# Optimization experiments

Measured on AMD Instinct MI355X. Metric: run time of the kernel, lower is better.

## Reference

```python
import jax, jax.numpy as jnp
import numpy as np

E, H, NH, FFN, OUT = 4096, 512, 4, 1024, 1
HD = H // NH
LN_EPS = 1e-5


def setup_inputs() -> dict:
    key = jax.random.key(0)
    ks = jax.random.split(key, 20)
    s = 1.0 / np.sqrt(H)
    inp = {
        'x': jax.random.normal(ks[0], (E, H), jnp.float32),
        'edge_index': jax.random.randint(ks[1], (2, E), 0, E, jnp.int64),
        # DMPNN message linear
        'W_msg': jax.random.normal(ks[2], (H, H), jnp.float32) * s,
        'b_msg': jnp.zeros((H,), jnp.float32),
        # GRUCell weights (torch layout: [3H, H], gates r,z,n)
        'W_ih': jax.random.normal(ks[3], (3 * H, H), jnp.float32) * s,
        'b_ih': jnp.zeros((3 * H,), jnp.float32),
        'W_hh': jax.random.normal(ks[4], (3 * H, H), jnp.float32) * s,
        'b_hh': jnp.zeros((3 * H,), jnp.float32),
        # MultiheadAttention combined in-proj [3H, H] and out-proj [H, H]
        'W_in_proj': jax.random.normal(ks[5], (3 * H, H), jnp.float32) * s,
        'b_in_proj': jnp.zeros((3 * H,), jnp.float32),
        'W_out_proj': jax.random.normal(ks[6], (H, H), jnp.float32) * s,
        'b_out_proj': jnp.zeros((H,), jnp.float32),
        # LayerNorm
        'ln_g': jnp.ones((H,), jnp.float32),
        'ln_b': jnp.zeros((H,), jnp.float32),
        # GlobalAttention output linear
        'W_lin': jax.random.normal(ks[7], (H, H), jnp.float32) * s,
        'b_lin': jnp.zeros((H,), jnp.float32),
        # FFN: Linear(H->FFN), ReLU, Linear(FFN->OUT)
        'W_f1': jax.random.normal(ks[8], (FFN, H), jnp.float32) * s,
        'b_f1': jnp.zeros((FFN,), jnp.float32),
        'W_f2': jax.random.normal(ks[9], (OUT, FFN), jnp.float32) * (1.0 / np.sqrt(FFN)),
        'b_f2': jnp.zeros((OUT,), jnp.float32),
    }
    return inp


def reference(x, edge_index, W_msg, b_msg, W_ih, b_ih, W_hh, b_hh,
              W_in_proj, b_in_proj, W_out_proj, b_out_proj, ln_g, ln_b,
              W_lin, b_lin, W_f1, b_f1, W_f2, b_f2):
    # ---- DMPNNLayer: message + scatter-add aggregation + GRUCell update ----
    msg = jax.nn.relu(x @ W_msg.T + b_msg)                       # [E, H]
    agg = jnp.zeros_like(x).at[edge_index[1]].add(msg)           # scatter-add to dst edges
    gi = agg @ W_ih.T + b_ih                                     # [E, 3H]
    gh = x @ W_hh.T + b_hh                                       # [E, 3H]
    ir, iz, inn = jnp.split(gi, 3, axis=-1)
    hr, hz, hn = jnp.split(gh, 3, axis=-1)
    r = jax.nn.sigmoid(ir + hr)
    z = jax.nn.sigmoid(iz + hz)
    n = jnp.tanh(inn + r * hn)
    h = (1.0 - z) * n + z * x                                    # [E, H] updated edges
    # ---- GlobalAttention: MHA(h,h,h) + residual LN + relu(linear) ----
    qkv = h @ W_in_proj.T + b_in_proj                            # [E, 3H]
    q, k, v = jnp.split(qkv, 3, axis=-1)
    split_heads = lambda t: t.reshape(E, NH, HD).transpose(1, 0, 2)  # [NH, E, HD]
    q, k, v = split_heads(q), split_heads(k), split_heads(v)
    scale = np.float32(1.0 / np.sqrt(HD))
    attn = jax.nn.softmax(jnp.einsum('hqd,hkd->hqk', q, k) * scale, axis=-1)
    o = jnp.einsum('hqk,hkd->hqd', attn, v).transpose(1, 0, 2).reshape(E, H)
    o = o @ W_out_proj.T + b_out_proj
    y = o + h
    mu = jnp.mean(y, axis=-1, keepdims=True)
    var = jnp.mean((y - mu) ** 2, axis=-1, keepdims=True)
    yn = (y - mu) / jnp.sqrt(var + LN_EPS) * ln_g + ln_b
    g = jax.nn.relu(yn @ W_lin.T + b_lin)                        # [E, H]
    # ---- FFN ----
    f = jax.nn.relu(g @ W_f1.T + b_f1)                           # [E, FFN]
    return f @ W_f2.T + b_f2                                     # [E, OUT]
```

## Files before the change

### kernel.cpp

```cpp
#include <hip/hip_runtime.h>

typedef unsigned short ushort_t;
typedef __attribute__((ext_vector_type(8))) short short8;
typedef __attribute__((ext_vector_type(4))) float float4v;

#define E_N   4096
#define H_N   512
#define NH_N  4
#define HD_N  128
#define FFN_N 1024
#define H3_N  1536

__device__ __forceinline__ float bf2f(ushort_t u) {
  union { unsigned u; float f; } v; v.u = ((unsigned)u) << 16; return v.f;
}
__device__ __forceinline__ ushort_t f2bf(float f) {
  union { float f; unsigned u; } v; v.f = f;
  unsigned r = v.u + 0x7fffu + ((v.u >> 16) & 1u);
  return (ushort_t)(r >> 16);
}
__device__ __forceinline__ uint4 cvt8(const float* p) {
  float4 a = *(const float4*)p;
  float4 b = *(const float4*)(p + 4);
  union { ushort_t u[8]; uint4 v; } pk;
  pk.u[0] = f2bf(a.x); pk.u[1] = f2bf(a.y); pk.u[2] = f2bf(a.z); pk.u[3] = f2bf(a.w);
  pk.u[4] = f2bf(b.x); pk.u[5] = f2bf(b.y); pk.u[6] = f2bf(b.z); pk.u[7] = f2bf(b.w);
  return pk.v;
}
__device__ __forceinline__ uint4 cvt8v(float4 a, float4 b) {
  union { ushort_t u[8]; uint4 v; } pk;
  pk.u[0] = f2bf(a.x); pk.u[1] = f2bf(a.y); pk.u[2] = f2bf(a.z); pk.u[3] = f2bf(a.w);
  pk.u[4] = f2bf(b.x); pk.u[5] = f2bf(b.y); pk.u[6] = f2bf(b.z); pk.u[7] = f2bf(b.w);
  return pk.v;
}

__device__ __forceinline__ void gload16(const void* g, void* l) {
  __builtin_amdgcn_global_load_lds(
      (const __attribute__((address_space(1))) unsigned*)g,
      (__attribute__((address_space(3))) unsigned*)l, 16, 0, 0);
}

__global__ __launch_bounds__(256) void prep_kernel(
    const float* __restrict__ wmsg, const float* __restrict__ wih,
    const float* __restrict__ whh,  const float* __restrict__ win,
    const float* __restrict__ wout, const float* __restrict__ wlin,
    const float* __restrict__ wf1,  ushort_t* __restrict__ wdst,
    float4* __restrict__ agg, const float* __restrict__ b2,
    float* __restrict__ out)
{
  int b = blockIdx.x;
  if (b < 2048) {
    agg[(size_t)b * 256 + threadIdx.x] = make_float4(0.f, 0.f, 0.f, 0.f);
    return;
  }
  if (b < 3840) {
    size_t o = ((size_t)(b - 2048) * 256 + threadIdx.x) * 8;
    const float* s;
    if      (o <  262144) s = wmsg + o;
    else if (o < 1048576) s = wih  + (o -  262144);
    else if (o < 1835008) s = whh  + (o - 1048576);
    else if (o < 2621440) s = win  + (o - 1835008);
    else if (o < 2883584) s = wout + (o - 2621440);
    else if (o < 3145728) s = wlin + (o - 2883584);
    else                  s = wf1  + (o - 3145728);
    *(uint4*)(wdst + o) = cvt8(s);
    return;
  }
  int i = (b - 3840) * 256 + threadIdx.x;
  out[i] = b2[0];
}

enum { MODE_MSG = 0, MODE_GI = 1, MODE_GH = 2, MODE_QKV = 3, MODE_OUT = 4,
       MODE_LIN = 5, MODE_F1 = 6 };

template <int MODE, int ASRC>
__global__ __launch_bounds__(256, 3) void gemm_bt(
    const void* __restrict__ Av, const ushort_t* __restrict__ W,
    const float* __restrict__ bias, int K,
    float* __restrict__ outf, ushort_t* __restrict__ outb,
    const int* __restrict__ edge, float* __restrict__ aggf,
    const ushort_t* __restrict__ hres,
    ushort_t* __restrict__ qb, ushort_t* __restrict__ kb,
    ushort_t* __restrict__ vt, const float* __restrict__ wf2)
{
  __shared__ ushort_t As[2][128 * 64];
  __shared__ ushort_t Bs[2][64 * 64];
  char* AsB = (char*)As;
  char* BsB = (char*)Bs;

  const int tid  = threadIdx.x;
  const int lane = tid & 63;
  const int wave = tid >> 6;
  const int quad = lane >> 4;
  const int l15  = lane & 15;
  const int m0 = blockIdx.x * 128;
  const int n0 = blockIdx.y * 64;
  const int wm = (wave >> 1) * 64;
  const int wn = (wave & 1) * 32;

  float4v acc[4][2];
#pragma unroll
  for (int i = 0; i < 4; i++)
#pragma unroll
    for (int j = 0; j < 2; j++)
#pragma unroll
      for (int r = 0; r < 4; r++) acc[i][j][r] = 0.f;

  const int ar = tid >> 3;
  const int ac = (tid & 7) * 8;
  const int awb = (ac * 2) ^ ((ar & 7) << 4);
  const int rmask = (l15 & 7) << 4;

  uint4  pa[4], pb[2];
  float4 fa[8];

#define LOADA(KK)                                                              \
  do {                                                                         \
    if constexpr (ASRC == 0) {                                                 \
      const ushort_t* Ab = (const ushort_t*)Av;                                \
      _Pragma("unroll")                                                        \
      for (int i = 0; i < 4; i++)                                              \
        pa[i] = *(const uint4*)(Ab + (size_t)(m0 + ar + 32 * i) * K + (KK) + ac); \
    } else {                                                                   \
      const float* Af = (const float*)Av;                                      \
      _Pragma("unroll")                                                        \
      for (int i = 0; i < 4; i++) {                                            \
        const float* p = Af + (size_t)(m0 + ar + 32 * i) * K + (KK) + ac;      \
        fa[2 * i]     = *(const float4*)(p);                                   \
        fa[2 * i + 1] = *(const float4*)(p + 4);                               \
      }                                                                        \
    }                                                                          \
  } while (0)

#define LOADB(KK)                                                              \
  do {                                                                         \
    _Pragma("unroll")                                                          \
    for (int i = 0; i < 2; i++)                                                \
      pb[i] = *(const uint4*)(W + (size_t)(n0 + ar + 32 * i) * K + (KK) + ac); \
  } while (0)

#define WRITEAB(BUF)                                                           \
  do {                                                                         \
    _Pragma("unroll")                                                          \
    for (int i = 0; i < 4; i++) {                                              \
      uint4 v_;                                                                \
      if constexpr (ASRC == 0) v_ = pa[i];                                     \
      else                     v_ = cvt8v(fa[2 * i], fa[2 * i + 1]);           \
      *(uint4*)(AsB + (BUF) * 16384 + (ar + 32 * i) * 128 + awb) = v_;         \
    }                                                                          \
    _Pragma("unroll")                                                          \
    for (int i = 0; i < 2; i++)                                                \
      *(uint4*)(BsB + (BUF) * 8192 + (ar + 32 * i) * 128 + awb) = pb[i];       \
  } while (0)

  LOADA(0);
  LOADB(0);
  WRITEAB(0);
  int cur = 0;

  for (int k0 = 0; k0 < K; k0 += 64) {
    const bool more = (k0 + 64 < K);
    if (more) { LOADA(k0 + 64); LOADB(k0 + 64); }
    __syncthreads();

#pragma unroll
    for (int ks = 0; ks < 2; ks++) {
      short8 af[4], bfr[2];
#pragma unroll
      for (int i = 0; i < 4; i++)
        af[i] = *(const short8*)(AsB + cur * 16384 +
                 (wm + i * 16 + l15) * 128 + ((ks * 64 + quad * 16) ^ rmask));
#pragma unroll
      for (int j = 0; j < 2; j++)
        bfr[j] = *(const short8*)(BsB + cur * 8192 +
                 (wn + j * 16 + l15) * 128 + ((ks * 64 + quad * 16) ^ rmask));
#pragma unroll
      for (int i = 0; i < 4; i++)
#pragma unroll
        for (int j = 0; j < 2; j++)
          acc[i][j] = __builtin_amdgcn_mfma_f32_16x16x32_bf16(af[i], bfr[j],
                                                              acc[i][j], 0, 0, 0);
    }

    if (more) WRITEAB(cur ^ 1);
    cur ^= 1;
  }
#undef LOADA
#undef LOADB
#undef WRITEAB

  if constexpr (MODE == MODE_F1) {
    float fsum[4][4];
#pragma unroll
    for (int i = 0; i < 4; i++)
#pragma unroll
      for (int r = 0; r < 4; r++) fsum[i][r] = 0.f;
#pragma unroll
    for (int j = 0; j < 2; j++) {
      const int col = n0 + wn + j * 16 + l15;
      const float bv = bias[col];
      const float wv = wf2[col];
#pragma unroll
      for (int i = 0; i < 4; i++)
#pragma unroll
        for (int r = 0; r < 4; r++)
          fsum[i][r] += fmaxf(acc[i][j][r] + bv, 0.f) * wv;
    }
#pragma unroll
    for (int i = 0; i < 4; i++)
#pragma unroll
      for (int r = 0; r < 4; r++) {
        float s = fsum[i][r];
        s += __shfl_xor(s, 1, 64); s += __shfl_xor(s, 2, 64);
        s += __shfl_xor(s, 4, 64); s += __shfl_xor(s, 8, 64);
        if (l15 == 0)
          atomicAdd(&outf[m0 + wm + i * 16 + quad * 4 + r], s);
      }
  } else {
#pragma unroll
    for (int j = 0; j < 2; j++) {
      const int col = n0 + wn + j * 16 + l15;
      const float bv = bias[col];
#pragma unroll
      for (int i = 0; i < 4; i++) {
#pragma unroll
        for (int r = 0; r < 4; r++) {
          const int row = m0 + wm + i * 16 + quad * 4 + r;
          float v = acc[i][j][r] + bv;
          if constexpr (MODE == MODE_MSG) {
            v = fmaxf(v, 0.f);
            const int dst = edge[E_N + row] & (E_N - 1);
            atomicAdd(&aggf[(size_t)dst * H_N + col], v);
          } else if constexpr (MODE == MODE_GI || MODE == MODE_GH) {
            outb[(size_t)row * H3_N + col] = f2bf(v);
          } else if constexpr (MODE == MODE_QKV) {
            const int part = col >> 9;
            const int hh   = (col >> 7) & 3;
            const int d    = col & 127;
            const ushort_t bvv = f2bf(v);
            if (part == 0)      qb[((size_t)hh * E_N + row) * HD_N + d] = bvv;
            else if (part == 1) kb[((size_t)hh * E_N + row) * HD_N + d] = bvv;
            else                vt[((size_t)hh * HD_N + d) * E_N + row] = bvv;
          } else if constexpr (MODE == MODE_OUT) {
            v += bf2f(hres[(size_t)row * H_N + col]);
            outf[(size_t)row * H_N + col] = v;
          } else {
            outb[(size_t)row * H_N + col] = f2bf(fmaxf(v, 0.f));
          }
        }
      }
    }
  }
}

__global__ __launch_bounds__(512, 2) void attn_kernel(
    const ushort_t* __restrict__ Qg, const ushort_t* __restrict__ Kg,
    const ushort_t* __restrict__ Vtg, ushort_t* __restrict__ Ob)
{
  const int bid  = blockIdx.x;
  const int head = bid & 3;
  const int qb0  = (bid >> 2) * 64;
  const int tid  = threadIdx.x;
  const int wave = tid >> 6;
  const int grp  = wave >> 2;
  const int w4   = wave & 3;
  const int lane = tid & 63;
  const int quad = lane >> 4;
  const int l15  = lane & 15;

  __shared__ ushort_t Ks[2][2][64][128];
  __shared__ ushort_t Vs[2][2][128][64];
  __shared__ ushort_t Ps[8][16][64];
  char* Psc = (char*)Ps + wave * 2048;

  const ushort_t* Qhead  = Qg  + (size_t)head * E_N * HD_N;
  const ushort_t* Khead  = Kg  + (size_t)head * E_N * HD_N;
  const ushort_t* Vthead = Vtg + (size_t)head * HD_N * E_N;

  short8 aq[4];
#pragma unroll
  for (int ks = 0; ks < 4; ks++)
    aq[ks] = *(const short8*)(Qhead +
        (size_t)(qb0 + w4 * 16 + l15) * HD_N + ks * 32 + quad * 8);

  float4v oacc[8];
#pragma unroll
  for (int i = 0; i < 8; i++)
#pragma unroll
    for (int r = 0; r < 4; r++) oacc[i][r] = 0.f;
  float mprev[4], lsum[4];
#pragma unroll
  for (int r = 0; r < 4; r++) { mprev[r] = -1e30f; lsum[r] = 0.f; }

  const float scale = 0.088388347648318447f;
  const int q15sw = (l15 & 7) << 4;

  const int kt0 = grp * 2048;

#define ISSUE(KT, BUF)                                                         \
  do {                                                                         \
    char* kb_ = (char*)Ks + ((grp * 2 + (BUF)) << 14);                         \
    char* vb_ = (char*)Vs + ((grp * 2 + (BUF)) << 14);                         \
    _Pragma("unroll")                                                          \
    for (int i_ = 0; i_ < 4; i_++) {                                           \
      const int c_ = w4 * 4 + i_;                                              \
      const int krow_ = 4 * c_ + (lane >> 4);              \
      gload16(Khead + (size_t)((KT) + krow_) * HD_N +                          \
                  (((((lane & 15) * 16)) ^ ((krow_ & 7) << 4)) >> 1),          \
              kb_ + c_ * 1024);                                                \
      const int vrow_ = 8 * c_ + (lane >> 3);             \
      gload16(Vthead + (size_t)vrow_ * E_N + (KT) +                            \
                  (((((lane & 7) * 16)) ^ ((lane >> 3) << 4)) >> 1),           \
              vb_ + c_ * 1024);                                                \
    }                                                                          \
  } while (0)

  ISSUE(kt0, 0);
  int cur = 0;

  for (int it = 0; it < 32; it++) {
    __syncthreads();
    if (it + 1 < 32) ISSUE(kt0 + (it + 1) * 64, cur ^ 1);

    const char* kt_ = (char*)Ks + ((grp * 2 + cur) << 14);
    const char* vt_ = (char*)Vs + ((grp * 2 + cur) << 14);

    float4v sacc[4];
#pragma unroll
    for (int j = 0; j < 4; j++)
#pragma unroll
      for (int r = 0; r < 4; r++) sacc[j][r] = 0.f;
#pragma unroll
    for (int ks = 0; ks < 4; ks++) {
#pragma unroll
      for (int j = 0; j < 4; j++) {
        short8 bk = *(const short8*)(kt_ + (j * 16 + l15) * 256 +
                                     ((ks * 64 + quad * 16) ^ q15sw));
        sacc[j] = __builtin_amdgcn_mfma_f32_16x16x32_bf16(aq[ks], bk, sacc[j], 0, 0, 0);
      }
    }

    float alpha[4], pv[4][4];
#pragma unroll
    for (int r = 0; r < 4; r++) {
      float mx = -1e30f;
#pragma unroll
      for (int j = 0; j < 4; j++) { float s = sacc[j][r] * scale; pv[j][r] = s; mx = fmaxf(mx, s); }
#pragma unroll
      for (int off = 1; off < 16; off <<= 1) mx = fmaxf(mx, __shfl_xor(mx, off, 64));
      float mnew = fmaxf(mprev[r], mx);
      alpha[r] = __expf(mprev[r] - mnew);
      float ss = 0.f;
#pragma unroll
      for (int j = 0; j < 4; j++) { float p = __expf(pv[j][r] - mnew); pv[j][r] = p; ss += p; }
#pragma unroll
      for (int off = 1; off < 16; off <<= 1) ss += __shfl_xor(ss, off, 64);
      lsum[r] = lsum[r] * alpha[r] + ss;
      mprev[r] = mnew;
    }
#pragma unroll
    for (int i = 0; i < 8; i++)
#pragma unroll
      for (int r = 0; r < 4; r++) oacc[i][r] *= alpha[r];

#pragma unroll
    for (int j = 0; j < 4; j++)
#pragma unroll
      for (int r = 0; r < 4; r++) {
        const int prow = quad * 4 + r;
        *(ushort_t*)(Psc + prow * 128 +
                     ((2 * (j * 16 + l15)) ^ ((prow & 7) << 4))) = f2bf(pv[j][r]);
      }

#pragma unroll
    for (int ks2 = 0; ks2 < 2; ks2++) {
      short8 ap = *(const short8*)(Psc + l15 * 128 +
                                   ((ks2 * 64 + quad * 16) ^ q15sw));
#pragma unroll
      for (int j = 0; j < 8; j++) {
        short8 bv = *(const short8*)(vt_ + (j * 16 + l15) * 128 +
                                     ((ks2 * 64 + quad * 16) ^ q15sw));
        oacc[j] = __builtin_amdgcn_mfma_f32_16x16x32_bf16(ap, bv, oacc[j], 0, 0, 0);
      }
    }
    cur ^= 1;
  }
#undef ISSUE

  __syncthreads();
  float* mO  = (float*)Ks;
  float* mML = (float*)Vs;
  if (grp == 1) {
#pragma unroll
    for (int j = 0; j < 8; j++)
#pragma unroll
      for (int r = 0; r < 4; r++)
        mO[(w4 * 16 + quad * 4 + r) * 128 + j * 16 + l15] = oacc[j][r];
    if (l15 == 0) {
#pragma unroll
      for (int r = 0; r < 4; r++) {
        mML[(w4 * 16 + quad * 4 + r) * 2 + 0] = mprev[r];
        mML[(w4 * 16 + quad * 4 + r) * 2 + 1] = lsum[r];
      }
    }
  }
  __syncthreads();
  if (grp == 0) {
    float s0[4], s1[4];
#pragma unroll
    for (int r = 0; r < 4; r++) {
      int rr = w4 * 16 + quad * 4 + r;
      float m1 = mML[rr * 2 + 0], l1 = mML[rr * 2 + 1];
      float m  = fmaxf(mprev[r], m1);
      float e0 = __expf(mprev[r] - m);
      float e1 = __expf(m1 - m);
      float inv = 1.f / (lsum[r] * e0 + l1 * e1);
      s0[r] = e0 * inv;
      s1[r] = e1 * inv;
    }
#pragma unroll
    for (int j = 0; j < 8; j++)
#pragma unroll
      for (int r = 0; r < 4; r++) {
        int row = qb0 + w4 * 16 + quad * 4 + r;
        int col = head * HD_N + j * 16 + l15;
        float o1 = mO[(w4 * 16 + quad * 4 + r) * 128 + j * 16 + l15];
        Ob[(size_t)row * H_N + col] = f2bf(oacc[j][r] * s0[r] + o1 * s1[r]);
      }
  }
}

__global__ __launch_bounds__(256) void gru_kernel(
    const ushort_t* __restrict__ gib, const ushort_t* __restrict__ ghb,
    const float* __restrict__ x, ushort_t* __restrict__ hb) {
  int t = blockIdx.x * 256 + threadIdx.x;
  int e = t >> 6, j8 = (t & 63) * 8;
  size_t b = (size_t)e * H3_N + j8;
  short8 vir = *(const short8*)(gib + b);
  short8 viz = *(const short8*)(gib + b + 512);
  short8 vin = *(const short8*)(gib + b + 1024);
  short8 vhr = *(const short8*)(ghb + b);
  short8 vhz = *(const short8*)(ghb + b + 512);
  short8 vhn = *(const short8*)(ghb + b + 1024);
  size_t xo = (size_t)e * H_N + j8;
  float4 x0 = *(const float4*)(x + xo);
  float4 x1 = *(const float4*)(x + xo + 4);
  float xv[8] = {x0.x, x0.y, x0.z, x0.w, x1.x, x1.y, x1.z, x1.w};
  union { ushort_t u[8]; uint4 v; } o;
#pragma unroll
  for (int i = 0; i < 8; i++) {
    float ir = bf2f((ushort_t)vir[i]), iz = bf2f((ushort_t)viz[i]), inn = bf2f((ushort_t)vin[i]);
    float hr = bf2f((ushort_t)vhr[i]), hz = bf2f((ushort_t)vhz[i]), hn  = bf2f((ushort_t)vhn[i]);
    float r = 1.f / (1.f + __expf(-(ir + hr)));
    float z = 1.f / (1.f + __expf(-(iz + hz)));
    float n = tanhf(inn + r * hn);
    o.u[i] = f2bf((1.f - z) * n + z * xv[i]);
  }
  *(uint4*)(hb + xo) = o.v;
}

__global__ __launch_bounds__(256) void ln_kernel(
    const float* __restrict__ y, const float* __restrict__ g,
    const float* __restrict__ b, ushort_t* __restrict__ yn) {
  int wave = threadIdx.x >> 6, lane = threadIdx.x & 63;
  int row = blockIdx.x * 4 + wave;
  const float* yr = y + (size_t)row * H_N;
  float v[8], s = 0.f;
#pragma unroll
  for (int i = 0; i < 8; i++) { v[i] = yr[lane + i * 64]; s += v[i]; }
#pragma unroll
  for (int off = 1; off < 64; off <<= 1) s += __shfl_xor(s, off, 64);
  float mu = s * (1.f / 512.f);
  float q = 0.f;
#pragma unroll
  for (int i = 0; i < 8; i++) { float d = v[i] - mu; q += d * d; }
#pragma unroll
  for (int off = 1; off < 64; off <<= 1) q += __shfl_xor(q, off, 64);
  float rstd = rsqrtf(q * (1.f / 512.f) + 1e-5f);
#pragma unroll
  for (int i = 0; i < 8; i++) {
    int c = lane + i * 64;
    yn[(size_t)row * H_N + c] = f2bf((v[i] - mu) * rstd * g[c] + b[c]);
  }
}

extern "C" void kernel_launch(void* const* d_in, const int* in_sizes, int n_in,
                              void* d_out, int out_size, void* d_ws, size_t ws_size,
                              hipStream_t stream) {
  const float* x     = (const float*)d_in[0];
  const int*   edge  = (const int*)d_in[1];
  const float* W_msg = (const float*)d_in[2];
  const float* b_msg = (const float*)d_in[3];
  const float* W_ih  = (const float*)d_in[4];
  const float* b_ih  = (const float*)d_in[5];
  const float* W_hh  = (const float*)d_in[6];
  const float* b_hh  = (const float*)d_in[7];
  const float* W_in  = (const float*)d_in[8];
  const float* b_in  = (const float*)d_in[9];
  const float* W_out = (const float*)d_in[10];
  const float* b_out = (const float*)d_in[11];
  const float* ln_g  = (const float*)d_in[12];
  const float* ln_b  = (const float*)d_in[13];
  const float* W_lin = (const float*)d_in[14];
  const float* b_lin = (const float*)d_in[15];
  const float* W_f1  = (const float*)d_in[16];
  const float* b_f1  = (const float*)d_in[17];
  const float* W_f2  = (const float*)d_in[18];
  const float* b_f2  = (const float*)d_in[19];

  char* ws = (char*)d_ws;
  const size_t MB = 1024 * 1024;
  float*    agg = (float*)(ws + 1 * MB);
  ushort_t* hb  = (ushort_t*)(ws + 1 * MB);
  ushort_t* gib = (ushort_t*)(ws + 9 * MB);
  ushort_t* ghb = (ushort_t*)(ws + 21 * MB);
  ushort_t* Qb  = (ushort_t*)(ws + 5 * MB);
  ushort_t* Kb  = (ushort_t*)(ws + 9 * MB);
  ushort_t* Vt  = (ushort_t*)(ws + 13 * MB);
  ushort_t* ob  = (ushort_t*)(ws + 17 * MB);
  float*    y   = (float*)(ws + 21 * MB);
  ushort_t* ynb = (ushort_t*)(ws + 29 * MB);
  ushort_t* gb  = (ushort_t*)(ws + 31 * MB);
  ushort_t* wbf = (ushort_t*)(ws + 33 * MB);
  ushort_t* Wmsg_b = wbf;
  ushort_t* Wih_b  = wbf + 262144;
  ushort_t* Whh_b  = wbf + 1048576;
  ushort_t* Win_b  = wbf + 1835008;
  ushort_t* Wout_b = wbf + 2621440;
  ushort_t* Wlin_b = wbf + 2883584;
  ushort_t* Wf1_b  = wbf + 3145728;

  prep_kernel<<<3856, 256, 0, stream>>>(
      W_msg, W_ih, W_hh, W_in, W_out, W_lin, W_f1, wbf,
      (float4*)agg, b_f2, (float*)d_out);

  gemm_bt<MODE_MSG, 1><<<dim3(32, 8), 256, 0, stream>>>(
      x, Wmsg_b, b_msg, H_N, nullptr, nullptr, edge, agg, nullptr,
      nullptr, nullptr, nullptr, nullptr);

  gemm_bt<MODE_GI, 1><<<dim3(32, 24), 256, 0, stream>>>(
      agg, Wih_b, b_ih, H_N, nullptr, gib, nullptr, nullptr, nullptr,
      nullptr, nullptr, nullptr, nullptr);

  gemm_bt<MODE_GH, 1><<<dim3(32, 24), 256, 0, stream>>>(
      x, Whh_b, b_hh, H_N, nullptr, ghb, nullptr, nullptr, nullptr,
      nullptr, nullptr, nullptr, nullptr);

  gru_kernel<<<1024, 256, 0, stream>>>(gib, ghb, x, hb);

  gemm_bt<MODE_QKV, 0><<<dim3(32, 24), 256, 0, stream>>>(
      hb, Win_b, b_in, H_N, nullptr, nullptr, nullptr, nullptr, nullptr,
      Qb, Kb, Vt, nullptr);

  attn_kernel<<<256, 512, 0, stream>>>(Qb, Kb, Vt, ob);

  gemm_bt<MODE_OUT, 0><<<dim3(32, 8), 256, 0, stream>>>(
      ob, Wout_b, b_out, H_N, y, nullptr, nullptr, nullptr, hb,
      nullptr, nullptr, nullptr, nullptr);

  ln_kernel<<<1024, 256, 0, stream>>>(y, ln_g, ln_b, ynb);

  gemm_bt<MODE_LIN, 0><<<dim3(32, 8), 256, 0, stream>>>(
      ynb, Wlin_b, b_lin, H_N, nullptr, gb, nullptr, nullptr, nullptr,
      nullptr, nullptr, nullptr, nullptr);

  gemm_bt<MODE_F1, 0><<<dim3(32, 16), 256, 0, stream>>>(
      gb, Wf1_b, b_f1, H_N, (float*)d_out, nullptr, nullptr, nullptr, nullptr,
      nullptr, nullptr, nullptr, W_f2);
}
```

Measured before the change: 340.3 us.

## Stage GEMM tiles via direct global-to-LDS loads with bf16 A inputs and BM=64 tiles

The GEMM now loads tiles with global_load_lds straight into swizzled LDS instead of going through registers. For that to work, every A operand must already be bf16, so x is converted in the prep kernel and agg gets its own conversion kernel. The narrow-N GEMMs (msg, out, lin) switch to a 64-row tile with twice as many blocks to raise occupancy. The cost is an extra kernel launch and the extra conversion traffic for x and agg.

```diff
diff --git a/kernel.cpp b/kernel.cpp
--- a/kernel.cpp
+++ b/kernel.cpp
@@ -27,12 +27,6 @@
   pk.u[4] = f2bf(b.x); pk.u[5] = f2bf(b.y); pk.u[6] = f2bf(b.z); pk.u[7] = f2bf(b.w);
   return pk.v;
 }
-__device__ __forceinline__ uint4 cvt8v(float4 a, float4 b) {
-  union { ushort_t u[8]; uint4 v; } pk;
-  pk.u[0] = f2bf(a.x); pk.u[1] = f2bf(a.y); pk.u[2] = f2bf(a.z); pk.u[3] = f2bf(a.w);
-  pk.u[4] = f2bf(b.x); pk.u[5] = f2bf(b.y); pk.u[6] = f2bf(b.z); pk.u[7] = f2bf(b.w);
-  return pk.v;
-}
 
 __device__ __forceinline__ void gload16(const void* g, void* l) {
   __builtin_amdgcn_global_load_lds(
@@ -41,10 +35,11 @@
 }
 
 __global__ __launch_bounds__(256) void prep_kernel(
+    const float* __restrict__ x,
     const float* __restrict__ wmsg, const float* __restrict__ wih,
     const float* __restrict__ whh,  const float* __restrict__ win,
     const float* __restrict__ wout, const float* __restrict__ wlin,
-    const float* __restrict__ wf1,  ushort_t* __restrict__ wdst,
+    const float* __restrict__ wf1,  ushort_t* __restrict__ dst,
     float4* __restrict__ agg, const float* __restrict__ b2,
     float* __restrict__ out)
 {
@@ -53,29 +48,36 @@
     agg[(size_t)b * 256 + threadIdx.x] = make_float4(0.f, 0.f, 0.f, 0.f);
     return;
   }
-  if (b < 3840) {
+  if (b < 4864) {
     size_t o = ((size_t)(b - 2048) * 256 + threadIdx.x) * 8;
     const float* s;
-    if      (o <  262144) s = wmsg + o;
-    else if (o < 1048576) s = wih  + (o -  262144);
-    else if (o < 1835008) s = whh  + (o - 1048576);
-    else if (o < 2621440) s = win  + (o - 1835008);
-    else if (o < 2883584) s = wout + (o - 2621440);
-    else if (o < 3145728) s = wlin + (o - 2883584);
-    else                  s = wf1  + (o - 3145728);
-    *(uint4*)(wdst + o) = cvt8(s);
+    if      (o < 2097152) s = x    + o;
+    else if (o < 2359296) s = wmsg + (o - 2097152);
+    else if (o < 3145728) s = wih  + (o - 2359296);
+    else if (o < 3932160) s = whh  + (o - 3145728);
+    else if (o < 4718592) s = win  + (o - 3932160);
+    else if (o < 4980736) s = wout + (o - 4718592);
+    else if (o < 5242880) s = wlin + (o - 4980736);
+    else                  s = wf1  + (o - 5242880);
+    *(uint4*)(dst + o) = cvt8(s);
     return;
   }
-  int i = (b - 3840) * 256 + threadIdx.x;
+  int i = (b - 4864) * 256 + threadIdx.x;
   out[i] = b2[0];
+}
+
+__global__ __launch_bounds__(256) void cvt_agg_kernel(
+    const float* __restrict__ agg, ushort_t* __restrict__ aggb) {
+  size_t o = ((size_t)blockIdx.x * 256 + threadIdx.x) * 8;
+  *(uint4*)(aggb + o) = cvt8(agg + o);
 }
 
 enum { MODE_MSG = 0, MODE_GI = 1, MODE_GH = 2, MODE_QKV = 3, MODE_OUT = 4,
        MODE_LIN = 5, MODE_F1 = 6 };
 
-template <int MODE, int ASRC>
-__global__ __launch_bounds__(256, 3) void gemm_bt(
-    const void* __restrict__ Av, const ushort_t* __restrict__ W,
+template <int MODE, int BM>
+__global__ __launch_bounds__(256, (BM == 64 ? 2 : 3)) void gemm_bt(
+    const ushort_t* __restrict__ A, const ushort_t* __restrict__ W,
     const float* __restrict__ bias, int K,
     float* __restrict__ outf, ushort_t* __restrict__ outb,
     const int* __restrict__ edge, float* __restrict__ aggf,
@@ -83,116 +85,87 @@
     ushort_t* __restrict__ qb, ushort_t* __restrict__ kb,
     ushort_t* __restrict__ vt, const float* __restrict__ wf2)
 {
-  __shared__ ushort_t As[2][128 * 64];
+  constexpr int MI   = BM / 32;
+  constexpr int ASZ  = BM * 128;
+  constexpr int BSZ  = 64 * 128;
+  constexpr int NCHA = BM / 8;
+  constexpr int NCH  = NCHA + 8;
+
+  __shared__ ushort_t As[2][BM * 64];
   __shared__ ushort_t Bs[2][64 * 64];
-  char* AsB = (char*)As;
-  char* BsB = (char*)Bs;
 
   const int tid  = threadIdx.x;
   const int lane = tid & 63;
   const int wave = tid >> 6;
   const int quad = lane >> 4;
   const int l15  = lane & 15;
-  const int m0 = blockIdx.x * 128;
+  const int m0 = blockIdx.x * BM;
   const int n0 = blockIdx.y * 64;
-  const int wm = (wave >> 1) * 64;
+  const int wm = (wave >> 1) * (BM / 2);
   const int wn = (wave & 1) * 32;
-
-  float4v acc[4][2];
-#pragma unroll
-  for (int i = 0; i < 4; i++)
+  const int rmask = (l15 & 7) << 4;
+
+  const int crow  = lane >> 3;
+  const int selem = ((((lane & 7) * 16)) ^ (crow << 4)) >> 1;
+
+  float4v acc[MI][2];
+#pragma unroll
+  for (int i = 0; i < MI; i++)
 #pragma unroll
     for (int j = 0; j < 2; j++)
 #pragma unroll
       for (int r = 0; r < 4; r++) acc[i][j][r] = 0.f;
 
-  const int ar = tid >> 3;
-  const int ac = (tid & 7) * 8;
-  const int awb = (ac * 2) ^ ((ar & 7) << 4);
-  const int rmask = (l15 & 7) << 4;
-
-  uint4  pa[4], pb[2];
-  float4 fa[8];
-
-#define LOADA(KK)                                                              \
+#define ISSUE(KK, BUF)                                                         \
   do {                                                                         \
-    if constexpr (ASRC == 0) {                                                 \
-      const ushort_t* Ab = (const ushort_t*)Av;                                \
-      _Pragma("unroll")                                                        \
-      for (int i = 0; i < 4; i++)                                              \
-        pa[i] = *(const uint4*)(Ab + (size_t)(m0 + ar + 32 * i) * K + (KK) + ac); \
-    } else {                                                                   \
-      const float* Af = (const float*)Av;                                      \
-      _Pragma("unroll")                                                        \
-      for (int i = 0; i < 4; i++) {                                            \
-        const float* p = Af + (size_t)(m0 + ar + 32 * i) * K + (KK) + ac;      \
-        fa[2 * i]     = *(const float4*)(p);                                   \
-        fa[2 * i + 1] = *(const float4*)(p + 4);                               \
+    _Pragma("unroll")                                                          \
+    for (int j_ = 0; j_ < NCH / 4; j_++) {                                     \
+      const int c_ = wave + j_ * 4;                                            \
+      if (c_ < NCHA) {                                                         \
+        const int row_ = c_ * 8 + crow;                                        \
+        gload16(A + (size_t)(m0 + row_) * K + (KK) + selem,                    \
+                (char*)As + (BUF) * ASZ + c_ * 1024);                          \
+      } else {                                                                 \
+        const int row_ = (c_ - NCHA) * 8 + crow;                               \
+        gload16(W + (size_t)(n0 + row_) * K + (KK) + selem,                    \
+                (char*)Bs + (BUF) * BSZ + (c_ - NCHA) * 1024);                 \
       }                                                                        \
     }                                                                          \
   } while (0)
 
-#define LOADB(KK)                                                              \
-  do {                                                                         \
-    _Pragma("unroll")                                                          \
-    for (int i = 0; i < 2; i++)                                                \
-      pb[i] = *(const uint4*)(W + (size_t)(n0 + ar + 32 * i) * K + (KK) + ac); \
-  } while (0)
-
-#define WRITEAB(BUF)                                                           \
-  do {                                                                         \
-    _Pragma("unroll")                                                          \
-    for (int i = 0; i < 4; i++) {                                              \
-      uint4 v_;                                                                \
-      if constexpr (ASRC == 0) v_ = pa[i];                                     \
-      else                     v_ = cvt8v(fa[2 * i], fa[2 * i + 1]);           \
-      *(uint4*)(AsB + (BUF) * 16384 + (ar + 32 * i) * 128 + awb) = v_;         \
-    }                                                                          \
-    _Pragma("unroll")                                                          \
-    for (int i = 0; i < 2; i++)                                                \
-      *(uint4*)(BsB + (BUF) * 8192 + (ar + 32 * i) * 128 + awb) = pb[i];       \
-  } while (0)
-
-  LOADA(0);
-  LOADB(0);
-  WRITEAB(0);
+  ISSUE(0, 0);
   int cur = 0;
 
   for (int k0 = 0; k0 < K; k0 += 64) {
-    const bool more = (k0 + 64 < K);
-    if (more) { LOADA(k0 + 64); LOADB(k0 + 64); }
     __syncthreads();
+    if (k0 + 64 < K) ISSUE(k0 + 64, cur ^ 1);
 
 #pragma unroll
     for (int ks = 0; ks < 2; ks++) {
-      short8 af[4], bfr[2];
-#pragma unroll
-      for (int i = 0; i < 4; i++)
-        af[i] = *(const short8*)(AsB + cur * 16384 +
+      short8 af[MI], bfr[2];
+#pragma unroll
+      for (int i = 0; i < MI; i++)
+        af[i] = *(const short8*)((char*)As + cur * ASZ +
                  (wm + i * 16 + l15) * 128 + ((ks * 64 + quad * 16) ^ rmask));
 #pragma unroll
       for (int j = 0; j < 2; j++)
-        bfr[j] = *(const short8*)(BsB + cur * 8192 +
+        bfr[j] = *(const short8*)((char*)Bs + cur * BSZ +
                  (wn + j * 16 + l15) * 128 + ((ks * 64 + quad * 16) ^ rmask));
 #pragma unroll
-      for (int i = 0; i < 4; i++)
+      for (int i = 0; i < MI; i++)
 #pragma unroll
         for (int j = 0; j < 2; j++)
           acc[i][j] = __builtin_amdgcn_mfma_f32_16x16x32_bf16(af[i], bfr[j],
                                                               acc[i][j], 0, 0, 0);
     }
-
-    if (more) WRITEAB(cur ^ 1);
     cur ^= 1;
   }
-#undef LOADA
-#undef LOADB
-#undef WRITEAB
+#undef ISSUE
 
   if constexpr (MODE == MODE_F1) {
-    float fsum[4][4];
-#pragma unroll
-    for (int i = 0; i < 4; i++)
+    float fsum[MI][4];
+#pragma unroll
+    for (int i = 0; i < MI; i++)
 #pragma unroll
       for (int r = 0; r < 4; r++) fsum[i][r] = 0.f;
 #pragma unroll
@@ -201,13 +174,13 @@
       const float bv = bias[col];
       const float wv = wf2[col];
 #pragma unroll
-      for (int i = 0; i < 4; i++)
+      for (int i = 0; i < MI; i++)
 #pragma unroll
         for (int r = 0; r < 4; r++)
           fsum[i][r] += fmaxf(acc[i][j][r] + bv, 0.f) * wv;
     }
 #pragma unroll
-    for (int i = 0; i < 4; i++)
+    for (int i = 0; i < MI; i++)
 #pragma unroll
       for (int r = 0; r < 4; r++) {
         float s = fsum[i][r];
@@ -222,7 +195,7 @@
       const int col = n0 + wn + j * 16 + l15;
       const float bv = bias[col];
 #pragma unroll
-      for (int i = 0; i < 4; i++) {
+      for (int i = 0; i < MI; i++) {
 #pragma unroll
         for (int r = 0; r < 4; r++) {
           const int row = m0 + wm + i * 16 + quad * 4 + r;
@@ -510,61 +483,64 @@
 
   char* ws = (char*)d_ws;
   const size_t MB = 1024 * 1024;
-  float*    agg = (float*)(ws + 1 * MB);
-  ushort_t* hb  = (ushort_t*)(ws + 1 * MB);
-  ushort_t* gib = (ushort_t*)(ws + 9 * MB);
-  ushort_t* ghb = (ushort_t*)(ws + 21 * MB);
-  ushort_t* Qb  = (ushort_t*)(ws + 5 * MB);
-  ushort_t* Kb  = (ushort_t*)(ws + 9 * MB);
-  ushort_t* Vt  = (ushort_t*)(ws + 13 * MB);
-  ushort_t* ob  = (ushort_t*)(ws + 17 * MB);
-  float*    y   = (float*)(ws + 21 * MB);
-  ushort_t* ynb = (ushort_t*)(ws + 29 * MB);
-  ushort_t* gb  = (ushort_t*)(ws + 31 * MB);
-  ushort_t* wbf = (ushort_t*)(ws + 33 * MB);
-  ushort_t* Wmsg_b = wbf;
-  ushort_t* Wih_b  = wbf + 262144;
-  ushort_t* Whh_b  = wbf + 1048576;
-  ushort_t* Win_b  = wbf + 1835008;
-  ushort_t* Wout_b = wbf + 2621440;
-  ushort_t* Wlin_b = wbf + 2883584;
-  ushort_t* Wf1_b  = wbf + 3145728;
-
-  prep_kernel<<<3856, 256, 0, stream>>>(
-      W_msg, W_ih, W_hh, W_in, W_out, W_lin, W_f1, wbf,
+  float*    agg  = (float*)(ws + 1 * MB);
+  ushort_t* hb   = (ushort_t*)(ws + 1 * MB);
+  ushort_t* gib  = (ushort_t*)(ws + 9 * MB);
+  ushort_t* ghb  = (ushort_t*)(ws + 21 * MB);
+  ushort_t* Qb   = (ushort_t*)(ws + 5 * MB);
+  ushort_t* Kb   = (ushort_t*)(ws + 9 * MB);
+  ushort_t* Vt   = (ushort_t*)(ws + 13 * MB);
+  ushort_t* ob   = (ushort_t*)(ws + 17 * MB);
+  float*    y    = (float*)(ws + 21 * MB);
+  ushort_t* ynb  = (ushort_t*)(ws + 29 * MB);
+  ushort_t* gb   = (ushort_t*)(ws + 31 * MB);
+  ushort_t* aggb = (ushort_t*)(ws + 29 * MB);
+  ushort_t* xb   = (ushort_t*)(ws + 33 * MB);
+  ushort_t* Wmsg_b = xb + 2097152;
+  ushort_t* Wih_b  = xb + 2359296;
+  ushort_t* Whh_b  = xb + 3145728;
+  ushort_t* Win_b  = xb + 3932160;
+  ushort_t* Wout_b = xb + 4718592;
+  ushort_t* Wlin_b = xb + 4980736;
+  ushort_t* Wf1_b  = xb + 5242880;
+
+  prep_kernel<<<4880, 256, 0, stream>>>(
+      x, W_msg, W_ih, W_hh, W_in, W_out, W_lin, W_f1, xb,
       (float4*)agg, b_f2, (float*)d_out);
 
-  gemm_bt<MODE_MSG, 1><<<dim3(32, 8), 256, 0, stream>>>(
-      x, Wmsg_b, b_msg, H_N, nullptr, nullptr, edge, agg, nullptr,
+  gemm_bt<MODE_MSG, 64><<<dim3(64, 8), 256, 0, stream>>>(
+      xb, Wmsg_b, b_msg, H_N, nullptr, nullptr, edge, agg, nullptr,
       nullptr, nullptr, nullptr, nullptr);
 
-  gemm_bt<MODE_GI, 1><<<dim3(32, 24), 256, 0, stream>>>(
-      agg, Wih_b, b_ih, H_N, nullptr, gib, nullptr, nullptr, nullptr,
+  cvt_agg_kernel<<<1024, 256, 0, stream>>>(agg, aggb);
+
+  gemm_bt<MODE_GI, 128><<<dim3(32, 24), 256, 0, stream>>>(
+      aggb, Wih_b, b_ih, H_N, nullptr, gib, nullptr, nullptr, nullptr,
       nullptr, nullptr, nullptr, nullptr);
 
-  gemm_bt<MODE_GH, 1><<<dim3(32, 24), 256, 0, stream>>>(
-      x, Whh_b, b_hh, H_N, nullptr, ghb, nullptr, nullptr, nullptr,
+  gemm_bt<MODE_GH, 128><<<dim3(32, 24), 256, 0, stream>>>(
+      xb, Whh_b, b_hh, H_N, nullptr, ghb, nullptr, nullptr, nullptr,
       nullptr, nullptr, nullptr, nullptr);
 
   gru_kernel<<<1024, 256, 0, stream>>>(gib, ghb, x, hb);
 
-  gemm_bt<MODE_QKV, 0><<<dim3(32, 24), 256, 0, stream>>>(
+  gemm_bt<MODE_QKV, 128><<<dim3(32, 24), 256, 0, stream>>>(
       hb, Win_b, b_in, H_N, nullptr, nullptr, nullptr, nullptr, nullptr,
       Qb, Kb, Vt, nullptr);
 
   attn_kernel<<<256, 512, 0, stream>>>(Qb, Kb, Vt, ob);
 
-  gemm_bt<MODE_OUT, 0><<<dim3(32, 8), 256, 0, stream>>>(
+  gemm_bt<MODE_OUT, 64><<<dim3(64, 8), 256, 0, stream>>>(
       ob, Wout_b, b_out, H_N, y, nullptr, nullptr, nullptr, hb,
       nullptr, nullptr, nullptr, nullptr);
 
   ln_kernel<<<1024, 256, 0, stream>>>(y, ln_g, ln_b, ynb);
 
-  gemm_bt<MODE_LIN, 0><<<dim3(32, 8), 256, 0, stream>>>(
+  gemm_bt<MODE_LIN, 64><<<dim3(64, 8), 256, 0, stream>>>(
       ynb, Wlin_b, b_lin, H_N, nullptr, gb, nullptr, nullptr, nullptr,
       nullptr, nullptr, nullptr, nullptr);
 
-  gemm_bt<MODE_F1, 0><<<dim3(32, 16), 256, 0, stream>>>(
+  gemm_bt<MODE_F1, 128><<<dim3(32, 16), 256, 0, stream>>>(
       gb, Wf1_b, b_f1, H_N, (float*)d_out, nullptr, nullptr, nullptr, nullptr,
       nullptr, nullptr, nullptr, W_f2);
 }
```

New measurement: 288.3 us. -15.3%, faster.
